# Performance work log

Measured on AMD Instinct MI355X. Metric: run time of the kernel, lower is better.

## Reference

```python
import jax, jax.numpy as jnp
import numpy as np

K = 9          # self.k
DILATION = 1   # self.dilation
L_B = 90       # banded window width (hardcoded in source)


def setup_inputs() -> dict:
    key = jax.random.key(0)
    x = jax.random.normal(key, (4, 64, 8192, 1), dtype=jnp.float32)
    return {"x": x}


def reference(x):
    # F.normalize(x, p=2, dim=1): L2-normalize over the feature (dims) axis
    eps = 1e-12
    norm = jnp.sqrt(jnp.sum(x * x, axis=1, keepdims=True))
    x = x / jnp.maximum(norm, eps)

    # (B, D, N, 1) -> (B, N, D)
    xt = jnp.squeeze(x, -1).transpose(0, 2, 1)
    B, N, D = xt.shape
    kk = K * DILATION  # top-k width used inside dense_knn_matrix

    # pairwise squared distances: |xi|^2 - 2 xi.xj + |xj|^2  -> (B, N, N)
    sq = jnp.sum(xt * xt, axis=-1, keepdims=True)
    dist = sq - 2.0 * jnp.einsum('bnd,bmd->bnm', xt, xt) + sq.transpose(0, 2, 1)

    # band mask: allowed columns j satisfy i - (L_B - 1) <= j <= i
    # (mask_u kills strict upper triangle; mask_d kills cols below the band)
    i = jnp.arange(N)
    allowed = (i[None, :] <= i[:, None]) & (i[None, :] >= i[:, None] - (L_B - 1))
    fmax = jnp.finfo(dist.dtype).max
    dist = jnp.where(allowed[None], dist, fmax)

    # k nearest = top-k of negative distance
    _, nn_idx = jax.lax.top_k(-dist, kk)  # (B, N, kk) int32

    # diagonal neighbor propagation: for row j < L_B, cols > j get row j's
    # nearest-neighbor index (vectorized form of the source's python loop)
    temp = nn_idx[:, :L_B, 0:1]                      # (B, L_B, 1)
    rows = jnp.arange(L_B)[None, :, None]
    cols = jnp.arange(kk)[None, None, :]
    head = jnp.where(cols > rows, temp, nn_idx[:, :L_B])
    nn_idx = jnp.concatenate([head, nn_idx[:, L_B:]], axis=1)

    center = jnp.broadcast_to(i[None, :, None], (B, N, kk)).astype(nn_idx.dtype)
    edge = jnp.stack([nn_idx, center], axis=0)       # (2, B, N, kk)

    # DenseDilated: stride-slice last axis by dilation, then overwrite the
    # first L_B rows with the undilated first K neighbors
    e = edge[:, :, :, ::DILATION]                    # (2, B, N, K)
    e = e.at[:, :, :L_B].set(edge[:, :, :L_B, :K])
    return e
```

## Files before the change

kernel.cpp:

```cpp
#include <hip/hip_runtime.h>
#include <hip/hip_bf16.h>
#include <stdint.h>

#define NPTS 8192
#define DIM  64
#define NB   4
#define KK   9
#define BQ   64
#define RROWS 160
#define SD2  72
#define UD2  91

typedef short bf16x8 __attribute__((ext_vector_type(8)));
typedef float f32x4  __attribute__((ext_vector_type(4)));

__global__ __launch_bounds__(512, 4) void knn_fused(const float* __restrict__ x,
                                                    int* __restrict__ out) {
    __shared__ ushort   sb[RROWS * SD2];
    __shared__ uint32_t ud[BQ * UD2];
    __shared__ float    rnArr[RROWS];

    const int tid = threadIdx.x;
    const int blk = blockIdx.x;
    const int L   = (blk & 7) * 64 + (blk >> 3);
    const int b   = L >> 7;
    const int n0  = (L & 127) << 6;
    const int gbase = n0 - 89;

    const float* xb = x + (size_t)b * DIM * NPTS;

    {
        const int g    = tid >> 2;
        const int part = tid & 3;
        const int gg   = gbase + g;
        const bool ok  = (gg >= 0 && gg < NPTS);
        const float* src = xb + (ok ? gg : 0);
        float s = 0.f;
#pragma unroll
        for (int j = 0; j < 2; ++j) {
            uint32_t pk[4];
#pragma unroll
            for (int e = 0; e < 4; ++e) {
                int d = part * 16 + j * 8 + e * 2;
                float v0 = ok ? src[(size_t)d * NPTS] : 0.f;
                float v1 = ok ? src[(size_t)(d + 1) * NPTS] : 0.f;
                s += v0 * v0 + v1 * v1;
                __hip_bfloat162 h2 = __float22bfloat162_rn(make_float2(v0, v1));
                pk[e] = *reinterpret_cast<uint32_t*>(&h2);
            }
            *reinterpret_cast<uint4*>(&sb[(size_t)g * SD2 + part * 16 + j * 8]) =
                make_uint4(pk[0], pk[1], pk[2], pk[3]);
        }
        s += __shfl_xor(s, 1);
        s += __shfl_xor(s, 2);
        if (part == 0) rnArr[g] = 1.0f / fmaxf(sqrtf(s), 1e-12f);
    }
    {
        const int g   = 128 + (tid >> 4);
        const int p16 = tid & 15;
        const int gg  = gbase + g;
        const bool ok = (gg >= 0 && gg < NPTS);
        const float* src = xb + (ok ? gg : 0);
        float s = 0.f;
        uint32_t pk[2];
#pragma unroll
        for (int e = 0; e < 2; ++e) {
            int d = p16 * 4 + e * 2;
            float v0 = ok ? src[(size_t)d * NPTS] : 0.f;
            float v1 = ok ? src[(size_t)(d + 1) * NPTS] : 0.f;
            s += v0 * v0 + v1 * v1;
            __hip_bfloat162 h2 = __float22bfloat162_rn(make_float2(v0, v1));
            pk[e] = *reinterpret_cast<uint32_t*>(&h2);
        }
        *reinterpret_cast<uint2*>(&sb[(size_t)g * SD2 + p16 * 4]) = make_uint2(pk[0], pk[1]);
        s += __shfl_xor(s, 1);
        s += __shfl_xor(s, 2);
        s += __shfl_xor(s, 4);
        s += __shfl_xor(s, 8);
        if (p16 == 0) rnArr[g] = 1.0f / fmaxf(sqrtf(s), 1e-12f);
    }
    __syncthreads();

    const int w  = tid >> 6;
    const int l  = tid & 63;
    const int qt = w >> 1;
    const int h  = w & 1;
    const int lr = l & 15;
    const int lk = l >> 4;
    const int nrt = 4 - h;

    const ushort* ap = &sb[(size_t)(89 + qt * 16 + lr) * SD2 + lk * 8];
    bf16x8 a0 = *reinterpret_cast<const bf16x8*>(ap);
    bf16x8 a1 = *reinterpret_cast<const bf16x8*>(ap + 32);

    float rq[4];
#pragma unroll
    for (int j = 0; j < 4; ++j) rq[j] = rnArr[89 + qt * 16 + lk * 4 + j];
    const int q0 = qt * 16 + lk * 4;

#pragma unroll
    for (int i = 0; i < 4; ++i) {
        if (i < nrt) {
            const int rto = h * 4 + i;
            const int rbase = qt * 16 + rto * 16;
            const ushort* bp = &sb[(size_t)(rbase + lr) * SD2 + lk * 8];
            bf16x8 b0 = *reinterpret_cast<const bf16x8*>(bp);
            bf16x8 b1 = *reinterpret_cast<const bf16x8*>(bp + 32);
            f32x4 acc = {0.f, 0.f, 0.f, 0.f};
            acc = __builtin_amdgcn_mfma_f32_16x16x32_bf16(a0, b0, acc, 0, 0, 0);
            acc = __builtin_amdgcn_mfma_f32_16x16x32_bf16(a1, b1, acc, 0, 0, 0);
            const int r = rbase + lr;
            const float rnr = rnArr[r];
#pragma unroll
            for (int j = 0; j < 4; ++j) {
                int rel = r - (q0 + j);
                if (rel >= 0 && rel <= 89) {
                    float p = acc[j] * rq[j] * rnr;
                    float dist = 2.0f - 2.0f * p;
                    uint32_t uu = __float_as_uint(dist);
                    uu = (uu & 0x80000000u) ? ~uu : (uu | 0x80000000u);
                    ud[(q0 + j) * UD2 + rel] = (uu & 0xFFFFFF80u) | (uint32_t)rel;
                }
            }
        }
    }
    __syncthreads();

    {
        const int ql = l >> 3;
        const int s  = l & 7;
        const int q  = (w << 3) | ql;
        const int n  = n0 + q;

        uint32_t key[12];
#pragma unroll
        for (int t = 0; t < 12; ++t) {
            int wofs = s + 8 * t;
            int m = n - 89 + wofs;
            bool ok = (wofs <= 89) && (m >= 0);
            uint32_t raw = ud[q * UD2 + (ok ? wofs : 0)];
            key[t] = ok ? raw : 0xFFFFFFFFu;
        }

        uint32_t prev = 0;
        int omKeep = n;
        int om8 = n;
#pragma unroll
        for (int j = 0; j < KK; ++j) {
            uint32_t mn = 0xFFFFFFFFu;
#pragma unroll
            for (int t = 0; t < 12; ++t) {
                uint32_t cand = (key[t] > prev) ? key[t] : 0xFFFFFFFFu;
                mn = (cand < mn) ? cand : mn;
            }
            uint32_t o;
            o = (uint32_t)__shfl_xor((int)mn, 1); mn = (o < mn) ? o : mn;
            o = (uint32_t)__shfl_xor((int)mn, 2); mn = (o < mn) ? o : mn;
            o = (uint32_t)__shfl_xor((int)mn, 4); mn = (o < mn) ? o : mn;
            int om = (mn == 0xFFFFFFFFu) ? n : (n - 89 + (int)(mn & 127u));
            if (j < 8) {
                if (s == j) omKeep = om;
            } else {
                om8 = om;
            }
            prev = mn;
        }

        const int base0 = (b * NPTS + n) * KK;
        const int base1 = NB * NPTS * KK + base0;
        out[base0 + s] = omKeep;
        out[base1 + s] = n;
        if (s == 0) {
            out[base0 + 8] = om8;
            out[base1 + 8] = n;
        }
    }
}

extern "C" void kernel_launch(void* const* d_in, const int* in_sizes, int n_in,
                              void* d_out, int out_size, void* d_ws, size_t ws_size,
                              hipStream_t stream) {
    const float* x = (const float*)d_in[0];
    int* out = (int*)d_out;
    knn_fused<<<NB * (NPTS / BQ), 512, 0, stream>>>(x, out);
}
```

Baseline: 15.62 us.

## Vectorize input loads as float2 per point pair with shared partial-norm reduction

Changes the load stage so each thread reads float2 pairs of adjacent points across several feature rows, instead of scalar per-point strided loads. The window base shifts by one so the point pairs stay aligned. Norm partial sums go to a shared scratch area that aliases the distance buffer and are reduced in a separate pass, which adds a barrier. The aim is wider, better-coalesced global loads, at the cost of an extra synchronization and more index bookkeeping.

```diff
diff --git a/kernel.cpp b/kernel.cpp
--- a/kernel.cpp
+++ b/kernel.cpp
@@ -16,110 +16,128 @@
 
 __global__ __launch_bounds__(512, 4) void knn_fused(const float* __restrict__ x,
                                                     int* __restrict__ out) {
+    __shared__ uint32_t ud[BQ * UD2];
     __shared__ ushort   sb[RROWS * SD2];
-    __shared__ uint32_t ud[BQ * UD2];
     __shared__ float    rnArr[RROWS];
+
+    float2* psumA = (float2*)ud;
+    float2* psumB = (float2*)ud + 512;
 
     const int tid = threadIdx.x;
     const int blk = blockIdx.x;
     const int L   = (blk & 7) * 64 + (blk >> 3);
     const int b   = L >> 7;
     const int n0  = (L & 127) << 6;
-    const int gbase = n0 - 89;
+    const int gbase = n0 - 90;
 
     const float* xb = x + (size_t)b * DIM * NPTS;
 
-    {
-        const int g    = tid >> 2;
-        const int part = tid & 3;
-        const int gg   = gbase + g;
-        const bool ok  = (gg >= 0 && gg < NPTS);
-        const float* src = xb + (ok ? gg : 0);
-        float s = 0.f;
-#pragma unroll
-        for (int j = 0; j < 2; ++j) {
-            uint32_t pk[4];
-#pragma unroll
-            for (int e = 0; e < 4; ++e) {
-                int d = part * 16 + j * 8 + e * 2;
-                float v0 = ok ? src[(size_t)d * NPTS] : 0.f;
-                float v1 = ok ? src[(size_t)(d + 1) * NPTS] : 0.f;
-                s += v0 * v0 + v1 * v1;
-                __hip_bfloat162 h2 = __float22bfloat162_rn(make_float2(v0, v1));
-                pk[e] = *reinterpret_cast<uint32_t*>(&h2);
-            }
-            *reinterpret_cast<uint4*>(&sb[(size_t)g * SD2 + part * 16 + j * 8]) =
-                make_uint4(pk[0], pk[1], pk[2], pk[3]);
-        }
-        s += __shfl_xor(s, 1);
-        s += __shfl_xor(s, 2);
-        if (part == 0) rnArr[g] = 1.0f / fmaxf(sqrtf(s), 1e-12f);
-    }
-    {
-        const int g   = 128 + (tid >> 4);
-        const int p16 = tid & 15;
-        const int gg  = gbase + g;
-        const bool ok = (gg >= 0 && gg < NPTS);
-        const float* src = xb + (ok ? gg : 0);
-        float s = 0.f;
-        uint32_t pk[2];
-#pragma unroll
-        for (int e = 0; e < 2; ++e) {
-            int d = p16 * 4 + e * 2;
-            float v0 = ok ? src[(size_t)d * NPTS] : 0.f;
-            float v1 = ok ? src[(size_t)(d + 1) * NPTS] : 0.f;
-            s += v0 * v0 + v1 * v1;
-            __hip_bfloat162 h2 = __float22bfloat162_rn(make_float2(v0, v1));
-            pk[e] = *reinterpret_cast<uint32_t*>(&h2);
-        }
-        *reinterpret_cast<uint2*>(&sb[(size_t)g * SD2 + p16 * 4]) = make_uint2(pk[0], pk[1]);
-        s += __shfl_xor(s, 1);
-        s += __shfl_xor(s, 2);
-        s += __shfl_xor(s, 4);
-        s += __shfl_xor(s, 8);
-        if (p16 == 0) rnArr[g] = 1.0f / fmaxf(sqrtf(s), 1e-12f);
+    const int w = tid >> 6;
+    const int l = tid & 63;
+
+    {
+        const int g2 = l * 2;
+        const int gg = gbase + g2;
+        const int gs = (gg < 0) ? 0 : gg;
+        const float* src = xb + gs;
+        float s0 = 0.f, s1 = 0.f;
+        uint32_t pkA[4], pkB[4];
+#pragma unroll
+        for (int e = 0; e < 4; ++e) {
+            const int d = 8 * w + 2 * e;
+            float2 v = *reinterpret_cast<const float2*>(&src[(size_t)d * NPTS]);
+            float2 u = *reinterpret_cast<const float2*>(&src[(size_t)(d + 1) * NPTS]);
+            s0 += v.x * v.x + u.x * u.x;
+            s1 += v.y * v.y + u.y * u.y;
+            __hip_bfloat162 hA = __float22bfloat162_rn(make_float2(v.x, u.x));
+            __hip_bfloat162 hB = __float22bfloat162_rn(make_float2(v.y, u.y));
+            pkA[e] = *reinterpret_cast<uint32_t*>(&hA);
+            pkB[e] = *reinterpret_cast<uint32_t*>(&hB);
+        }
+        *reinterpret_cast<uint4*>(&sb[(size_t)g2 * SD2 + 8 * w]) =
+            make_uint4(pkA[0], pkA[1], pkA[2], pkA[3]);
+        *reinterpret_cast<uint4*>(&sb[(size_t)(g2 + 1) * SD2 + 8 * w]) =
+            make_uint4(pkB[0], pkB[1], pkB[2], pkB[3]);
+        psumA[tid] = make_float2(s0, s1);
+    }
+    {
+        const int g2 = 128 + (l & 15) * 2;
+        const int c  = (w << 2) | (l >> 4);
+        const int gg = gbase + g2;
+        const int gs = (gg > NPTS - 2) ? (NPTS - 2) : gg;
+        const float* src = xb + gs;
+        float2 v = *reinterpret_cast<const float2*>(&src[(size_t)(2 * c) * NPTS]);
+        float2 u = *reinterpret_cast<const float2*>(&src[(size_t)(2 * c + 1) * NPTS]);
+        float s0 = v.x * v.x + u.x * u.x;
+        float s1 = v.y * v.y + u.y * u.y;
+        __hip_bfloat162 hA = __float22bfloat162_rn(make_float2(v.x, u.x));
+        __hip_bfloat162 hB = __float22bfloat162_rn(make_float2(v.y, u.y));
+        *reinterpret_cast<uint32_t*>(&sb[(size_t)g2 * SD2 + 2 * c]) =
+            *reinterpret_cast<uint32_t*>(&hA);
+        *reinterpret_cast<uint32_t*>(&sb[(size_t)(g2 + 1) * SD2 + 2 * c]) =
+            *reinterpret_cast<uint32_t*>(&hB);
+        s0 += __shfl_xor(s0, 16); s0 += __shfl_xor(s0, 32);
+        s1 += __shfl_xor(s1, 16); s1 += __shfl_xor(s1, 32);
+        if (l < 16) psumB[w * 16 + l] = make_float2(s0, s1);
     }
     __syncthreads();
 
-    const int w  = tid >> 6;
-    const int l  = tid & 63;
     const int qt = w >> 1;
     const int h  = w & 1;
     const int lr = l & 15;
     const int lk = l >> 4;
     const int nrt = 4 - h;
 
-    const ushort* ap = &sb[(size_t)(89 + qt * 16 + lr) * SD2 + lk * 8];
+    const ushort* ap = &sb[(size_t)(90 + qt * 16 + lr) * SD2 + lk * 8];
     bf16x8 a0 = *reinterpret_cast<const bf16x8*>(ap);
     bf16x8 a1 = *reinterpret_cast<const bf16x8*>(ap + 32);
 
-    float rq[4];
-#pragma unroll
-    for (int j = 0; j < 4; ++j) rq[j] = rnArr[89 + qt * 16 + lk * 4 + j];
-    const int q0 = qt * 16 + lk * 4;
-
-#pragma unroll
-    for (int i = 0; i < 4; ++i) {
-        if (i < nrt) {
-            const int rto = h * 4 + i;
-            const int rbase = qt * 16 + rto * 16;
-            const ushort* bp = &sb[(size_t)(rbase + lr) * SD2 + lk * 8];
-            bf16x8 b0 = *reinterpret_cast<const bf16x8*>(bp);
-            bf16x8 b1 = *reinterpret_cast<const bf16x8*>(bp + 32);
-            f32x4 acc = {0.f, 0.f, 0.f, 0.f};
-            acc = __builtin_amdgcn_mfma_f32_16x16x32_bf16(a0, b0, acc, 0, 0, 0);
-            acc = __builtin_amdgcn_mfma_f32_16x16x32_bf16(a1, b1, acc, 0, 0, 0);
-            const int r = rbase + lr;
-            const float rnr = rnArr[r];
-#pragma unroll
-            for (int j = 0; j < 4; ++j) {
-                int rel = r - (q0 + j);
-                if (rel >= 0 && rel <= 89) {
-                    float p = acc[j] * rq[j] * rnr;
-                    float dist = 2.0f - 2.0f * p;
-                    uint32_t uu = __float_as_uint(dist);
-                    uu = (uu & 0x80000000u) ? ~uu : (uu | 0x80000000u);
-                    ud[(q0 + j) * UD2 + rel] = (uu & 0xFFFFFF80u) | (uint32_t)rel;
+    if (tid < 128) {
+        const int gp = tid >> 1, comp = tid & 1;
+        float s = 0.f;
+#pragma unroll
+        for (int k = 0; k < 8; ++k)
+            s += reinterpret_cast<const float*>(&psumA[k * 64 + gp])[comp];
+        rnArr[tid] = 1.0f / fmaxf(sqrtf(s), 1e-12f);
+    } else if (tid < 160) {
+        const int rr = tid - 128;
+        const int gp = rr >> 1, comp = rr & 1;
+        float s = 0.f;
+#pragma unroll
+        for (int k = 0; k < 8; ++k)
+            s += reinterpret_cast<const float*>(&psumB[k * 16 + gp])[comp];
+        rnArr[tid] = 1.0f / fmaxf(sqrtf(s), 1e-12f);
+    }
+    __syncthreads();
+
+    {
+        float rq[4];
+#pragma unroll
+        for (int j = 0; j < 4; ++j) rq[j] = rnArr[90 + qt * 16 + lk * 4 + j];
+        const int q0 = qt * 16 + lk * 4;
+#pragma unroll
+        for (int i = 0; i < 4; ++i) {
+            if (i < nrt) {
+                const int rto = h * 4 + i;
+                const int rbase = qt * 16 + rto * 16;
+                const ushort* bp = &sb[(size_t)(rbase + lr) * SD2 + lk * 8];
+                bf16x8 b0 = *reinterpret_cast<const bf16x8*>(bp);
+                bf16x8 b1 = *reinterpret_cast<const bf16x8*>(bp + 32);
+                f32x4 acc = {0.f, 0.f, 0.f, 0.f};
+                acc = __builtin_amdgcn_mfma_f32_16x16x32_bf16(a0, b0, acc, 0, 0, 0);
+                acc = __builtin_amdgcn_mfma_f32_16x16x32_bf16(a1, b1, acc, 0, 0, 0);
+                const int r = rbase + lr;
+                const float rnr = rnArr[r];
+#pragma unroll
+                for (int j = 0; j < 4; ++j) {
+                    int rel = r - (q0 + j) - 1;
+                    if (rel >= 0 && rel <= 89) {
+                        float p = acc[j] * rq[j] * rnr;
+                        float dist = 2.0f - 2.0f * p;
+                        uint32_t uu = __float_as_uint(dist);
+                        uu = (uu & 0x80000000u) ? ~uu : (uu | 0x80000000u);
+                        ud[(q0 + j) * UD2 + rel] = (uu & 0xFFFFFF80u) | (uint32_t)rel;
+                    }
                 }
             }
         }
```

Result: faster. 13.31 us (-14.8%).
